# Kernel tuning notes

Measured on AMD Instinct MI355X. Metric: run time of the kernel, lower is better.

Reference implementation:

```python
import jax, jax.numpy as jnp
import numpy as np

NEG = -1e6  # mask fill value used by d2l.sequence_mask


def setup_inputs() -> dict:
    key = jax.random.key(0)
    k1, k2, k3, k4, k5, k6, k7 = jax.random.split(key, 7)
    B, Q, K, DQ, DK, H, DV = 8, 256, 1024, 256, 256, 128, 128
    queries = jax.random.normal(k1, (B, Q, DQ), dtype=jnp.float32)
    keys = jax.random.normal(k2, (B, K, DK), dtype=jnp.float32)
    values = jax.random.normal(k3, (B, K, DV), dtype=jnp.float32)
    valid_lens = jax.random.randint(k4, (B,), 1, K + 1, dtype=jnp.int32)
    # learned params (nn.Linear stores weight as [out, in]; apply as x @ W.T)
    W_q = jax.random.normal(k5, (H, DQ), dtype=jnp.float32) / np.sqrt(DQ)
    W_k = jax.random.normal(k6, (H, DK), dtype=jnp.float32) / np.sqrt(DK)
    w_v = jax.random.normal(k7, (H,), dtype=jnp.float32) / np.sqrt(H)
    return {"queries": queries, "keys": keys, "values": values,
            "valid_lens": valid_lens, "W_q": W_q, "W_k": W_k, "w_v": w_v}


def reference(queries, keys, values, valid_lens, W_q, W_k, w_v):
    # projections
    q = jnp.einsum('bqd,hd->bqh', queries, W_q)   # [B,Q,H]
    k = jnp.einsum('bkd,hd->bkh', keys, W_k)      # [B,K,H]
    # broadcast add + tanh -> [B,Q,K,H] (the fusion-headroom intermediate)
    features = jnp.tanh(q[:, :, None, :] + k[:, None, :, :])
    scores = jnp.einsum('bqkh,h->bqk', features, w_v)  # [B,Q,K]
    # masked softmax: valid_lens is per-batch (dim==1 path)
    klen = scores.shape[-1]
    mask = jnp.arange(klen)[None, None, :] < valid_lens[:, None, None]
    scores = jnp.where(mask, scores, NEG)
    weights = jax.nn.softmax(scores, axis=-1)
    # dropout is identity in eval mode
    return jnp.einsum('bqk,bkv->bqv', weights, values)
```

## Files before the change

### kernel.cpp

```cpp
#include <hip/hip_runtime.h>


#define Bb 8
#define Qn 256
#define Kk 1024
#define Dd 256
#define Hh 128
#define DVv 128

__device__ __forceinline__ float fexp2(float x) { return __builtin_amdgcn_exp2f(x); }
__device__ __forceinline__ float frcp(float x)  { return __builtin_amdgcn_rcpf(x); }

__global__ __launch_bounds__(256)
void repack_w(const float* __restrict__ Wq, const float* __restrict__ Wk,
              float4* __restrict__ Wq4T, float4* __restrict__ Wk4T)
{
    const int blk = blockIdx.x;
    const float* src = (blk < 32) ? Wq : Wk;
    float4*      dst = (blk < 32) ? Wq4T : Wk4T;
    const int idx = (blk & 31) * 256 + threadIdx.x;
    const int g = idx >> 7;
    const int h = idx & 127;
    dst[idx] = *(const float4*)(src + (size_t)h * Dd + g * 4);
}

__global__ __launch_bounds__(512)
void proj_exp_kernel(const float* __restrict__ queries,
                     const float* __restrict__ keys,
                     const float4* __restrict__ Wq4T,
                     const float4* __restrict__ Wk4T,
                     float* __restrict__ EqT,
                     float* __restrict__ EkT)
{
    __shared__ __align__(16) float Xs[16 * 256];
    const int blk = blockIdx.x;
    const float* X; const float4* W4; float* outT; int RB; int i0;
    if (blk < 128) { X = queries; W4 = Wq4T; outT = EqT; RB = Qn; i0 = blk * 16; }
    else           { X = keys;    W4 = Wk4T; outT = EkT; RB = Kk; i0 = (blk - 128) * 16; }
    const int tid = threadIdx.x;
    const int h   = tid & 127;
    const int r4  = __builtin_amdgcn_readfirstlane(tid >> 7);

    {
        const float4* xsrc = (const float4*)(X + (size_t)i0 * Dd);
#pragma unroll
        for (int s = 0; s < 2; ++s) {
            const int idx = tid + 512 * s;
            *(float4*)(Xs + idx * 4) = xsrc[idx];
        }
    }
    __syncthreads();

    float acc[4] = {0.f, 0.f, 0.f, 0.f};
    const float4* wp = W4 + h;
    const float*  xr = Xs + (r4 * 4) * 256;
#pragma unroll 8
    for (int g = 0; g < 64; ++g) {
        const float4 w = wp[(size_t)g * 128];
#pragma unroll
        for (int i = 0; i < 4; ++i) {
            const float4 x = *(const float4*)(xr + i * 256 + g * 4);
            acc[i] = fmaf(x.x, w.x, acc[i]);
            acc[i] = fmaf(x.y, w.y, acc[i]);
            acc[i] = fmaf(x.z, w.z, acc[i]);
            acc[i] = fmaf(x.w, w.w, acc[i]);
        }
    }
    const int b    = i0 / RB;
    const int rloc = (i0 % RB) + r4 * 4;
    float4 o;
    o.x = fexp2(acc[0] * 2.885390082f);
    o.y = fexp2(acc[1] * 2.885390082f);
    o.z = fexp2(acc[2] * 2.885390082f);
    o.w = fexp2(acc[3] * 2.885390082f);
    *(float4*)(outT + (size_t)b * Hh * RB + (size_t)h * RB + rloc) = o;
}

#define SCORE4(q4, w4, ea, eb, ec, ed, accref)                                \
    {                                                                          \
        const float A_ = fmaf((q4).x, (ea), 1.f), B_ = fmaf((q4).y, (eb), 1.f);\
        const float C_ = fmaf((q4).z, (ec), 1.f), E_ = fmaf((q4).w, (ed), 1.f);\
        const float AB_ = A_ * B_, CE_ = C_ * E_;                              \
        const float N_ = fmaf(fmaf((w4).x, B_, (w4).y * A_), CE_,              \
                              fmaf((w4).z, E_, (w4).w * C_) * AB_);            \
        (accref) = fmaf(N_, frcp(AB_ * CE_), (accref));                        \
    }

__global__ __launch_bounds__(512, 4)
void score_softmax_pv_kernel(const float* __restrict__ EqT,
                             const float* __restrict__ EkT,
                             const float* __restrict__ wv,
                             const int* __restrict__ valid_lens,
                             const float* __restrict__ values,
                             float* __restrict__ out)
{
    __shared__ __align__(16) float  s_sc[4][Kk];
    __shared__ __align__(16) float  eqsT[4][Hh];
    __shared__ __align__(16) float  w2s[Hh];
    __shared__ __align__(16) float4 s_part[7][4][32];
    __shared__ float s_qmax[4][2];
    __shared__ float s_qsum[4][2];

    const int blk  = blockIdx.x;
    const int b    = blk & 7;
    const int qt   = blk >> 3;
    const int q0   = qt * 4;
    const int len  = valid_lens[b];
    const int tid  = threadIdx.x;
    const int lane = tid & 63;
    const int wave = __builtin_amdgcn_readfirstlane(tid >> 6);

    if (tid < 128) {
        const float4 v = *(const float4*)(EqT + (size_t)b * Hh * Qn + (size_t)tid * Qn + q0);
        eqsT[0][tid] = v.x; eqsT[1][tid] = v.y; eqsT[2][tid] = v.z; eqsT[3][tid] = v.w;
    } else if (tid < 256) {
        w2s[tid - 128] = -2.0f * wv[tid - 128];
    }
    __syncthreads();

    {
        const float* ekh = EkT + (size_t)b * Hh * Kk + tid;
        if (len > 512) {
            float acc[4][2] = {};
#pragma unroll 2
            for (int hg = 0; hg < 32; ++hg) {
                const int h = hg << 2;
                const float* ep = ekh + (size_t)h * Kk;
                const float e00 = ep[0];
                const float e01 = ep[Kk];
                const float e02 = ep[2 * Kk];
                const float e03 = ep[3 * Kk];
                const float e10 = ep[512];
                const float e11 = ep[Kk + 512];
                const float e12 = ep[2 * Kk + 512];
                const float e13 = ep[3 * Kk + 512];
                const float4 w4 = *(const float4*)(w2s + h);
#pragma unroll
                for (int q = 0; q < 4; ++q) {
                    const float4 q4 = *(const float4*)(&eqsT[q][h]);
                    SCORE4(q4, w4, e00, e01, e02, e03, acc[q][0]);
                    SCORE4(q4, w4, e10, e11, e12, e13, acc[q][1]);
                }
            }
#pragma unroll
            for (int q = 0; q < 4; ++q) {
                s_sc[q][tid]       = acc[q][0];
                s_sc[q][tid + 512] = acc[q][1];
            }
        } else {
            float acc[4] = {};
#pragma unroll 2
            for (int hg = 0; hg < 32; ++hg) {
                const int h = hg << 2;
                const float* ep = ekh + (size_t)h * Kk;
                const float e00 = ep[0];
                const float e01 = ep[Kk];
                const float e02 = ep[2 * Kk];
                const float e03 = ep[3 * Kk];
                const float4 w4 = *(const float4*)(w2s + h);
#pragma unroll
                for (int q = 0; q < 4; ++q) {
                    const float4 q4 = *(const float4*)(&eqsT[q][h]);
                    SCORE4(q4, w4, e00, e01, e02, e03, acc[q]);
                }
            }
#pragma unroll
            for (int q = 0; q < 4; ++q) s_sc[q][tid] = acc[q];
        }
    }
    __syncthreads();

    {
        const int q    = wave & 3;
        const int half = wave >> 2;
        const int base = half * 512;
        const int hi   = (base + 512 < len) ? base + 512 : len;
        float m = -3.0e38f;
        for (int i = base + lane; i < hi; i += 64) m = fmaxf(m, s_sc[q][i]);
#pragma unroll
        for (int off = 32; off > 0; off >>= 1) m = fmaxf(m, __shfl_xor(m, off));
        if (lane == 0) s_qmax[q][half] = m;
        __syncthreads();
        const float gm = fmaxf(s_qmax[q][0], s_qmax[q][1]);
        float sum = 0.f;
        for (int i = base + lane; i < hi; i += 64) {
            const float p = fexp2((s_sc[q][i] - gm) * 1.44269504f);
            s_sc[q][i] = p;
            sum += p;
        }
#pragma unroll
        for (int off = 32; off > 0; off >>= 1) sum += __shfl_xor(sum, off);
        if (lane == 0) s_qsum[q][half] = sum;
    }
    __syncthreads();

    {
        const int slice = tid >> 5;
        const int l32   = tid & 31;
        const int v4    = l32 << 2;
        const float* vp = values + (size_t)b * Kk * DVv + v4;
        float a[4][4];
#pragma unroll
        for (int q = 0; q < 4; ++q) { a[q][0]=0.f; a[q][1]=0.f; a[q][2]=0.f; a[q][3]=0.f; }
        for (int k = slice; k < len; k += 16) {
            const float4 val = *(const float4*)(vp + (size_t)k * DVv);
            const float w0 = s_sc[0][k], w1 = s_sc[1][k], w2 = s_sc[2][k], w3 = s_sc[3][k];
            a[0][0] = fmaf(w0, val.x, a[0][0]);
            a[0][1] = fmaf(w0, val.y, a[0][1]);
            a[0][2] = fmaf(w0, val.z, a[0][2]);
            a[0][3] = fmaf(w0, val.w, a[0][3]);
            a[1][0] = fmaf(w1, val.x, a[1][0]);
            a[1][1] = fmaf(w1, val.y, a[1][1]);
            a[1][2] = fmaf(w1, val.z, a[1][2]);
            a[1][3] = fmaf(w1, val.w, a[1][3]);
            a[2][0] = fmaf(w2, val.x, a[2][0]);
            a[2][1] = fmaf(w2, val.y, a[2][1]);
            a[2][2] = fmaf(w2, val.z, a[2][2]);
            a[2][3] = fmaf(w2, val.w, a[2][3]);
            a[3][0] = fmaf(w3, val.x, a[3][0]);
            a[3][1] = fmaf(w3, val.y, a[3][1]);
            a[3][2] = fmaf(w3, val.z, a[3][2]);
            a[3][3] = fmaf(w3, val.w, a[3][3]);
        }
#pragma unroll
        for (int q = 0; q < 4; ++q)
#pragma unroll
            for (int x = 0; x < 4; ++x) a[q][x] += __shfl_xor(a[q][x], 32);
        if (wave > 0 && lane < 32) {
#pragma unroll
            for (int q = 0; q < 4; ++q)
                s_part[wave - 1][q][l32] = make_float4(a[q][0], a[q][1], a[q][2], a[q][3]);
        }
        __syncthreads();
        if (wave == 0 && lane < 32) {
#pragma unroll
            for (int q = 0; q < 4; ++q) {
                float r0 = a[q][0], r1 = a[q][1], r2 = a[q][2], r3 = a[q][3];
#pragma unroll
                for (int w = 0; w < 7; ++w) {
                    const float4 p = s_part[w][q][l32];
                    r0 += p.x; r1 += p.y; r2 += p.z; r3 += p.w;
                }
                const float inv = frcp(s_qsum[q][0] + s_qsum[q][1]);
                *(float4*)(out + (size_t)(b * Qn + q0 + q) * DVv + v4) =
                    make_float4(r0 * inv, r1 * inv, r2 * inv, r3 * inv);
            }
        }
    }
}

extern "C" void kernel_launch(void* const* d_in, const int* in_sizes, int n_in,
                              void* d_out, int out_size, void* d_ws, size_t ws_size,
                              hipStream_t stream) {
    (void)in_sizes; (void)n_in; (void)out_size; (void)ws_size;
    const float* queries    = (const float*)d_in[0];
    const float* keys       = (const float*)d_in[1];
    const float* values     = (const float*)d_in[2];
    const int*   valid_lens = (const int*)  d_in[3];
    const float* Wq         = (const float*)d_in[4];
    const float* Wk         = (const float*)d_in[5];
    const float* wvv        = (const float*)d_in[6];
    float* out = (float*)d_out;

    float* Wq4T = (float*)d_ws;
    float* Wk4T = Wq4T + (size_t)Dd * Hh;
    float* EqT  = Wk4T + (size_t)Dd * Hh;
    float* EkT  = EqT + (size_t)Bb * Hh * Qn;

    repack_w       <<<  64, 256, 0, stream>>>(Wq, Wk, (float4*)Wq4T, (float4*)Wk4T);
    proj_exp_kernel<<< 640, 512, 0, stream>>>(queries, keys, (const float4*)Wq4T,
                                              (const float4*)Wk4T, EqT, EkT);
    score_softmax_pv_kernel<<<512, 512, 0, stream>>>(EqT, EkT, wvv, valid_lens,
                                                     values, out);
}
```

Measured before the change: 135.3 us.

## Split score computation into separate finely-tiled kernel with early exit

Moves the tanh-score computation out of the fused softmax/PV kernel into its own kernel with 256-key tiles, storing scores to a global workspace buffer. Tiles lying beyond the batch's valid length exit immediately, so less masked work is done and more blocks are available to fill the GPU. In exchange the scores make a global memory round trip and there is an extra kernel launch.

Result: slower. 148.5 us (+9.8%).

```diff
diff --git a/kernel.cpp b/kernel.cpp
--- a/kernel.cpp
+++ b/kernel.cpp
@@ -86,87 +86,77 @@
         (accref) = fmaf(N_, frcp(AB_ * CE_), (accref));                        \
     }
 
+__global__ __launch_bounds__(256, 8)
+void score_kernel(const float* __restrict__ EqT,
+                  const float* __restrict__ EkT,
+                  const float* __restrict__ wv,
+                  const int* __restrict__ valid_lens,
+                  float* __restrict__ S)
+{
+    __shared__ __align__(16) float eqsT[4][Hh];
+    __shared__ __align__(16) float w2s[Hh];
+    const int blk = blockIdx.x;
+    const int b   = blk & 7;
+    const int kt  = (blk >> 3) & 3;
+    const int qt  = blk >> 5;
+    const int len = valid_lens[b];
+    if (kt * 256 >= len) return;
+
+    const int tid = threadIdx.x;
+    const int q0  = qt * 4;
+    if (tid < 128) {
+        const float4 v = *(const float4*)(EqT + (size_t)b * Hh * Qn + (size_t)tid * Qn + q0);
+        eqsT[0][tid] = v.x; eqsT[1][tid] = v.y; eqsT[2][tid] = v.z; eqsT[3][tid] = v.w;
+    } else {
+        w2s[tid - 128] = -2.0f * wv[tid - 128];
+    }
+    __syncthreads();
+
+    const int k = kt * 256 + tid;
+    const float* ekp = EkT + (size_t)b * Hh * Kk + k;
+    float a[4] = {0.f, 0.f, 0.f, 0.f};
+#pragma unroll 4
+    for (int hg = 0; hg < 32; ++hg) {
+        const int h = hg << 2;
+        const float e0 = ekp[(size_t)(h + 0) * Kk];
+        const float e1 = ekp[(size_t)(h + 1) * Kk];
+        const float e2 = ekp[(size_t)(h + 2) * Kk];
+        const float e3 = ekp[(size_t)(h + 3) * Kk];
+        const float4 w4 = *(const float4*)(w2s + h);
+#pragma unroll
+        for (int q = 0; q < 4; ++q) {
+            const float4 q4 = *(const float4*)(&eqsT[q][h]);
+            SCORE4(q4, w4, e0, e1, e2, e3, a[q]);
+        }
+    }
+    float* srow = S + (size_t)(b * Qn + q0) * Kk + k;
+#pragma unroll
+    for (int q = 0; q < 4; ++q) srow[(size_t)q * Kk] = a[q];
+}
+
 __global__ __launch_bounds__(512, 4)
-void score_softmax_pv_kernel(const float* __restrict__ EqT,
-                             const float* __restrict__ EkT,
-                             const float* __restrict__ wv,
-                             const int* __restrict__ valid_lens,
-                             const float* __restrict__ values,
-                             float* __restrict__ out)
+void softmax_pv_kernel(const float* __restrict__ S,
+                       const float* __restrict__ values,
+                       const int* __restrict__ valid_lens,
+                       float* __restrict__ out)
 {
     __shared__ __align__(16) float  s_sc[4][Kk];
-    __shared__ __align__(16) float  eqsT[4][Hh];
-    __shared__ __align__(16) float  w2s[Hh];
     __shared__ __align__(16) float4 s_part[7][4][32];
     __shared__ float s_qmax[4][2];
     __shared__ float s_qsum[4][2];
 
     const int blk  = blockIdx.x;
     const int b    = blk & 7;
-    const int qt   = blk >> 3;
-    const int q0   = qt * 4;
-    const int len  = valid_lens[b];
+    const int q0   = (blk >> 3) << 2;
     const int tid  = threadIdx.x;
     const int lane = tid & 63;
     const int wave = __builtin_amdgcn_readfirstlane(tid >> 6);
-
-    if (tid < 128) {
-        const float4 v = *(const float4*)(EqT + (size_t)b * Hh * Qn + (size_t)tid * Qn + q0);
-        eqsT[0][tid] = v.x; eqsT[1][tid] = v.y; eqsT[2][tid] = v.z; eqsT[3][tid] = v.w;
-    } else if (tid < 256) {
-        w2s[tid - 128] = -2.0f * wv[tid - 128];
-    }
-    __syncthreads();
-
-    {
-        const float* ekh = EkT + (size_t)b * Hh * Kk + tid;
-        if (len > 512) {
-            float acc[4][2] = {};
-#pragma unroll 2
-            for (int hg = 0; hg < 32; ++hg) {
-                const int h = hg << 2;
-                const float* ep = ekh + (size_t)h * Kk;
-                const float e00 = ep[0];
-                const float e01 = ep[Kk];
-                const float e02 = ep[2 * Kk];
-                const float e03 = ep[3 * Kk];
-                const float e10 = ep[512];
-                const float e11 = ep[Kk + 512];
-                const float e12 = ep[2 * Kk + 512];
-                const float e13 = ep[3 * Kk + 512];
-                const float4 w4 = *(const float4*)(w2s + h);
-#pragma unroll
-                for (int q = 0; q < 4; ++q) {
-                    const float4 q4 = *(const float4*)(&eqsT[q][h]);
-                    SCORE4(q4, w4, e00, e01, e02, e03, acc[q][0]);
-                    SCORE4(q4, w4, e10, e11, e12, e13, acc[q][1]);
-                }
-            }
-#pragma unroll
-            for (int q = 0; q < 4; ++q) {
-                s_sc[q][tid]       = acc[q][0];
-                s_sc[q][tid + 512] = acc[q][1];
-            }
-        } else {
-            float acc[4] = {};
-#pragma unroll 2
-            for (int hg = 0; hg < 32; ++hg) {
-                const int h = hg << 2;
-                const float* ep = ekh + (size_t)h * Kk;
-                const float e00 = ep[0];
-                const float e01 = ep[Kk];
-                const float e02 = ep[2 * Kk];
-                const float e03 = ep[3 * Kk];
-                const float4 w4 = *(const float4*)(w2s + h);
-#pragma unroll
-                for (int q = 0; q < 4; ++q) {
-                    const float4 q4 = *(const float4*)(&eqsT[q][h]);
-                    SCORE4(q4, w4, e00, e01, e02, e03, acc[q]);
-                }
-            }
-#pragma unroll
-            for (int q = 0; q < 4; ++q) s_sc[q][tid] = acc[q];
-        }
+    const int len  = valid_lens[b];
+
+#pragma unroll
+    for (int j = 0; j < 4; ++j) {
+        const float* sr = S + (size_t)(b * Qn + q0 + j) * Kk;
+        for (int k = tid; k < len; k += 512) s_sc[j][k] = sr[k];
     }
     __syncthreads();
 
@@ -266,10 +256,11 @@
     float* Wk4T = Wq4T + (size_t)Dd * Hh;
     float* EqT  = Wk4T + (size_t)Dd * Hh;
     float* EkT  = EqT + (size_t)Bb * Hh * Qn;
+    float* S    = EkT + (size_t)Bb * Hh * Kk;
 
     repack_w       <<<  64, 256, 0, stream>>>(Wq, Wk, (float4*)Wq4T, (float4*)Wk4T);
     proj_exp_kernel<<< 640, 512, 0, stream>>>(queries, keys, (const float4*)Wq4T,
                                               (const float4*)Wk4T, EqT, EkT);
-    score_softmax_pv_kernel<<<512, 512, 0, stream>>>(EqT, EkT, wvv, valid_lens,
-                                                     values, out);
-}
+    score_kernel   <<<2048, 256, 0, stream>>>(EqT, EkT, wvv, valid_lens, S);
+    softmax_pv_kernel<<<512, 512, 0, stream>>>(S, values, valid_lens, out);
+}
```
